# Kernel optimization log

Hardware: AMD Instinct MI355X
Metric: run time of the kernel (lower is better)

The kernel has to match this reference:

```python
import jax, jax.numpy as jnp
import numpy as np

T, B, E = 2048, 2, 256
H = 8
D = E // H


def setup_inputs() -> dict:
    key = jax.random.key(0)
    ks = jax.random.split(key, 10)
    s = 1.0 / np.sqrt(E)
    return {
        "query": jax.random.normal(ks[0], (T, B, E), jnp.float32),
        "attn_bias": jax.random.normal(ks[1], (B, T, T), jnp.float32),
        "Wq": jax.random.normal(ks[2], (E, E), jnp.float32) * s,
        "bq": jax.random.normal(ks[3], (E,), jnp.float32) * 0.02,
        "Wk": jax.random.normal(ks[4], (E, E), jnp.float32) * s,
        "bk": jax.random.normal(ks[5], (E,), jnp.float32) * 0.02,
        "Wv": jax.random.normal(ks[6], (E, E), jnp.float32) * s,
        "bv": jax.random.normal(ks[7], (E,), jnp.float32) * 0.02,
        "Wo": jax.random.normal(ks[8], (E, E), jnp.float32) * s,
        "bo": jax.random.normal(ks[9], (E,), jnp.float32) * 0.02,
    }


def reference(query, attn_bias, Wq, bq, Wk, bk, Wv, bv, Wo, bo):
    # query: [T, B, E] (seq-first). Self-attention: k,v also projected from query.
    t, b, e = query.shape
    scaling = 1.0 / np.sqrt(D)
    q = (query @ Wq.T + bq) * scaling          # [T,B,E]
    k = query @ Wk.T + bk                      # [T,B,E]
    v = query @ Wv.T + bv                      # [T,B,E]
    q = q.reshape(t, b, H, D)
    k = k.reshape(t, b, H, D)
    v = v.reshape(t, b, H, D)
    # raw scores + per-batch additive bias broadcast across heads
    scores = jnp.einsum("tbhd,sbhd->bhts", q, k) + attn_bias[:, None, :, :]
    attn_weights = jax.nn.softmax(scores, axis=-1)  # [B,H,T,S]
    attn = jnp.einsum("bhts,sbhd->tbhd", attn_weights, v).reshape(t, b, e)
    return attn @ Wo.T + bo  # [T,B,E]
```

## Files before the change

kernel.cpp:

```cpp
#include <hip/hip_runtime.h>
#include <hip/hip_bf16.h>

#define T_DIM 2048
#define B_DIM 2
#define E_DIM 256
#define H_DIM 8
#define D_DIM 32
#define M_DIM (T_DIM*B_DIM)
#define SPLIT 4
#define S_CHUNK (T_DIM/SPLIT)

typedef __bf16 bf16x8 __attribute__((ext_vector_type(8)));
typedef __bf16 bf16x4 __attribute__((ext_vector_type(4)));
typedef __bf16 bf16x2 __attribute__((ext_vector_type(2)));
typedef float  f32x4  __attribute__((ext_vector_type(4)));

static __device__ __forceinline__ float fexp2(float x) {
#if __has_builtin(__builtin_amdgcn_exp2f)
    return __builtin_amdgcn_exp2f(x);
#else
    return exp2f(x);
#endif
}

__global__ __launch_bounds__(256)
void qkv_kernel(const float* __restrict__ X,
                const float* __restrict__ Wq, const float* __restrict__ Wk, const float* __restrict__ Wv,
                const float* __restrict__ bq, const float* __restrict__ bk, const float* __restrict__ bv,
                __bf16* __restrict__ qh, __bf16* __restrict__ kperm, __bf16* __restrict__ vperm) {
    __shared__ __align__(16) __bf16 Xs[64][136];
    __shared__ __align__(16) __bf16 Ws[64][136];
    const int m0 = blockIdx.x * 64;
    const int which = blockIdx.y >> 2;
    const int n0 = (blockIdx.y & 3) * 64;
    const float* W = (which == 0) ? Wq : (which == 1) ? Wk : Wv;
    const float* bias = (which == 0) ? bq : (which == 1) ? bk : bv;
    const int tid = threadIdx.x;
    const int wid = tid >> 6, lane = tid & 63;
    const int wm = (wid & 1) * 32, wn = (wid >> 1) * 32;
    const int lr = lane & 15, lg = lane >> 4;

    f32x4 acc[2][2] = {};
    for (int kc = 0; kc < 2; ++kc) {
        for (int c = tid; c < 2048; c += 256) {
            int row = c >> 5, col = (c & 31) * 4;
            float4 xv = *(const float4*)&X[(size_t)(m0 + row) * E_DIM + kc * 128 + col];
            float4 wv = *(const float4*)&W[(size_t)(n0 + row) * E_DIM + kc * 128 + col];
            bf16x4 xb, wb;
            xb[0] = (__bf16)xv.x; xb[1] = (__bf16)xv.y; xb[2] = (__bf16)xv.z; xb[3] = (__bf16)xv.w;
            wb[0] = (__bf16)wv.x; wb[1] = (__bf16)wv.y; wb[2] = (__bf16)wv.z; wb[3] = (__bf16)wv.w;
            *(bf16x4*)&Xs[row][col] = xb;
            *(bf16x4*)&Ws[row][col] = wb;
        }
        __syncthreads();
#pragma unroll
        for (int ks = 0; ks < 4; ++ks) {
            bf16x8 a0 = *(const bf16x8*)&Xs[wm + lr][ks * 32 + lg * 8];
            bf16x8 a1 = *(const bf16x8*)&Xs[wm + 16 + lr][ks * 32 + lg * 8];
            bf16x8 b0 = *(const bf16x8*)&Ws[wn + lr][ks * 32 + lg * 8];
            bf16x8 b1 = *(const bf16x8*)&Ws[wn + 16 + lr][ks * 32 + lg * 8];
            acc[0][0] = __builtin_amdgcn_mfma_f32_16x16x32_bf16(a0, b0, acc[0][0], 0, 0, 0);
            acc[0][1] = __builtin_amdgcn_mfma_f32_16x16x32_bf16(a0, b1, acc[0][1], 0, 0, 0);
            acc[1][0] = __builtin_amdgcn_mfma_f32_16x16x32_bf16(a1, b0, acc[1][0], 0, 0, 0);
            acc[1][1] = __builtin_amdgcn_mfma_f32_16x16x32_bf16(a1, b1, acc[1][1], 0, 0, 0);
        }
        __syncthreads();
    }
    const float scale = 0.17677669529663687f * 1.4426950408889634f;
#pragma unroll
    for (int mt = 0; mt < 2; ++mt) {
#pragma unroll
        for (int nt = 0; nt < 2; ++nt) {
            int n = n0 + wn + nt * 16 + lr;
            float bb = bias[n];
            int h = n >> 5, d = n & 31;
#pragma unroll
            for (int r = 0; r < 4; ++r) {
                int m = m0 + wm + mt * 16 + lg * 4 + r;
                int t = m >> 1, b = m & 1;
                float v = acc[mt][nt][r] + bb;
                if (which == 0) {
                    v *= scale;
                    qh[((size_t)(b * H_DIM + h) * T_DIM + t) * D_DIM + d] = (__bf16)v;
                } else if (which == 1) {
                    int til = t >> 6, s6 = t & 63;
                    int ntk = ((s6 >> 5) << 1) | ((s6 >> 2) & 1);
                    int lrk = (((s6 >> 3) & 3) << 2) | (s6 & 3);
                    int lanek = ((d >> 3) << 4) | lrk;
                    kperm[((((size_t)(b * H_DIM + h) * 32 + til) * 4 + ntk) * 64 + lanek) * 8 + (d & 7)] = (__bf16)v;
                } else {
                    int til = t >> 6;
                    int ktv = (t >> 5) & 1, lgv = (t >> 3) & 3, elv = t & 7;
                    int jv = ktv * 2 + (d >> 4);
                    int lanev = (lgv << 4) | (d & 15);
                    vperm[((((size_t)(b * H_DIM + h) * 32 + til) * 4 + jv) * 64 + lanev) * 8 + elv] = (__bf16)v;
                }
            }
        }
    }
}

__global__ __launch_bounds__(512, 4)
void attn_kernel(const __bf16* __restrict__ qh, const __bf16* __restrict__ kperm,
                 const __bf16* __restrict__ vperm, const float* __restrict__ attn_bias,
                 __bf16* __restrict__ po, float* __restrict__ pl) {
    __shared__ __align__(16) float Bs[16][516];
    const int lin = blockIdx.x + (T_DIM / 16) * (blockIdx.y + B_DIM * blockIdx.z);
    const int combo = lin & 7;
    const int b  = combo & 1;
    const int sp = combo >> 1;
    const int t0 = (lin >> 3) * 16;
    const int tid = threadIdx.x, wid = tid >> 6, lane = tid & 63;
    const int lr = lane & 15, lg = lane >> 4;
    const int bh = b * H_DIM + wid;
    const int sbase = sp * S_CHUNK;
    const int tb0 = sp * 8;
    const float LOG2E = 1.4426950408889634f;

    {
        const float* bsrc = attn_bias + ((size_t)b * T_DIM + t0) * T_DIM + sbase;
        int r = tid >> 5, c0 = (tid & 31) * 4;
#pragma unroll
        for (int rep = 0; rep < 4; ++rep) {
            float4 v = *(const float4*)&bsrc[(size_t)r * T_DIM + rep * 128 + c0];
            float4 w;
            w.x = (v.x - 12.0f) * LOG2E;
            w.y = (v.y - 12.0f) * LOG2E;
            w.z = (v.z - 12.0f) * LOG2E;
            w.w = (v.w - 12.0f) * LOG2E;
            *(float4*)&Bs[r][rep * 128 + c0] = w;
        }
    }
    __syncthreads();

    bf16x8 qf = *(const bf16x8*)&qh[((size_t)bh * T_DIM + t0 + lr) * D_DIM + lg * 8];
    const __bf16* kpb = kperm + (size_t)bh * T_DIM * D_DIM + (size_t)lane * 8;
    const __bf16* vpb = vperm + (size_t)bh * T_DIM * D_DIM + (size_t)lane * 8;

    bf16x8 ones;
#pragma unroll
    for (int i = 0; i < 8; ++i) ones[i] = (__bf16)1.0f;

    f32x4 o0 = {}, o1 = {};
    f32x4 ol = {};

#pragma unroll
    for (int st = 0; st < 8; ++st) {
        const int til = tb0 + st;

        bf16x8 kf0 = *(const bf16x8*)&kpb[(size_t)(til * 4 + 0) * 512];
        bf16x8 kf1 = *(const bf16x8*)&kpb[(size_t)(til * 4 + 1) * 512];
        bf16x8 kf2 = *(const bf16x8*)&kpb[(size_t)(til * 4 + 2) * 512];
        bf16x8 kf3 = *(const bf16x8*)&kpb[(size_t)(til * 4 + 3) * 512];
        bf16x8 vf0 = *(const bf16x8*)&vpb[(size_t)(til * 4 + 0) * 512];
        bf16x8 vf1 = *(const bf16x8*)&vpb[(size_t)(til * 4 + 1) * 512];
        bf16x8 vf2 = *(const bf16x8*)&vpb[(size_t)(til * 4 + 2) * 512];
        bf16x8 vf3 = *(const bf16x8*)&vpb[(size_t)(til * 4 + 3) * 512];

        f32x4 cb0 = *(const f32x4*)&Bs[lr][st * 64 +  0 + lg * 8 + 0];
        f32x4 cb1 = *(const f32x4*)&Bs[lr][st * 64 +  0 + lg * 8 + 4];
        f32x4 cb2 = *(const f32x4*)&Bs[lr][st * 64 + 32 + lg * 8 + 0];
        f32x4 cb3 = *(const f32x4*)&Bs[lr][st * 64 + 32 + lg * 8 + 4];

        f32x4 sv0 = __builtin_amdgcn_mfma_f32_16x16x32_bf16(kf0, qf, cb0, 0, 0, 0);
        f32x4 sv1 = __builtin_amdgcn_mfma_f32_16x16x32_bf16(kf1, qf, cb1, 0, 0, 0);
        f32x4 sv2 = __builtin_amdgcn_mfma_f32_16x16x32_bf16(kf2, qf, cb2, 0, 0, 0);
        f32x4 sv3 = __builtin_amdgcn_mfma_f32_16x16x32_bf16(kf3, qf, cb3, 0, 0, 0);

        f32x4 e0, e1, e2, e3;
#pragma unroll
        for (int r = 0; r < 4; ++r) {
            e0[r] = fexp2(sv0[r]);
            e1[r] = fexp2(sv1[r]);
            e2[r] = fexp2(sv2[r]);
            e3[r] = fexp2(sv3[r]);
        }

        bf16x8 pf0, pf1;
#pragma unroll
        for (int r = 0; r < 4; ++r) {
            pf0[r] = (__bf16)e0[r]; pf0[4 + r] = (__bf16)e1[r];
            pf1[r] = (__bf16)e2[r]; pf1[4 + r] = (__bf16)e3[r];
        }

        o0 = __builtin_amdgcn_mfma_f32_16x16x32_bf16(pf0, vf0, o0, 0, 0, 0);
        o1 = __builtin_amdgcn_mfma_f32_16x16x32_bf16(pf0, vf1, o1, 0, 0, 0);
        ol = __builtin_amdgcn_mfma_f32_16x16x32_bf16(pf0, ones, ol, 0, 0, 0);
        o0 = __builtin_amdgcn_mfma_f32_16x16x32_bf16(pf1, vf2, o0, 0, 0, 0);
        o1 = __builtin_amdgcn_mfma_f32_16x16x32_bf16(pf1, vf3, o1, 0, 0, 0);
        ol = __builtin_amdgcn_mfma_f32_16x16x32_bf16(pf1, ones, ol, 0, 0, 0);
    }

#pragma unroll
    for (int r = 0; r < 4; ++r) {
        int t = t0 + lg * 4 + r;
        size_t rw = ((size_t)bh * T_DIM + t) * SPLIT + sp;
        bf16x2 w;
        w[0] = (__bf16)o0[r];
        w[1] = (__bf16)o1[r];
        *(bf16x2*)&po[rw * D_DIM + lr * 2] = w;
    }
    if (lr == 0)
        *(f32x4*)&pl[(size_t)sp * (B_DIM * H_DIM * T_DIM) + (size_t)bh * T_DIM + t0 + lg * 4] = ol;
}

__global__ __launch_bounds__(256)
void combine_kernel(const __bf16* __restrict__ po, const float* __restrict__ pl,
                    __bf16* __restrict__ attn) {
    int idx = blockIdx.x * 256 + threadIdx.x;
    int row = idx >> 3, dg = idx & 7;
    int bh = row >> 11, t = row & 2047;
    int b = bh >> 3, h = bh & 7;

    float L = 0.f;
    float a0 = 0.f, a1 = 0.f, b0 = 0.f, b1 = 0.f;
#pragma unroll
    for (int s2 = 0; s2 < SPLIT; ++s2) {
        L += pl[(size_t)s2 * (B_DIM * H_DIM * T_DIM) + row];
        bf16x4 v = *(const bf16x4*)&po[((size_t)row * SPLIT + s2) * D_DIM + dg * 4];
        a0 += (float)v[0];
        b0 += (float)v[1];
        a1 += (float)v[2];
        b1 += (float)v[3];
    }
    float inv = 1.0f / L;
    bf16x2 lo, hi;
    lo[0] = (__bf16)(a0 * inv); lo[1] = (__bf16)(a1 * inv);
    hi[0] = (__bf16)(b0 * inv); hi[1] = (__bf16)(b1 * inv);
    size_t base = ((size_t)(t * B_DIM + b)) * E_DIM + h * D_DIM;
    *(bf16x2*)&attn[base + 2 * dg] = lo;
    *(bf16x2*)&attn[base + 16 + 2 * dg] = hi;
}

__global__ __launch_bounds__(256)
void oproj_kernel(const __bf16* __restrict__ X, const float* __restrict__ Wo,
                  const float* __restrict__ bo, float* __restrict__ out) {
    __shared__ __align__(16) __bf16 Xs[64][136];
    __shared__ __align__(16) __bf16 Ws[64][136];
    const int m0 = blockIdx.x * 64;
    const int n0 = blockIdx.y * 64;
    const int tid = threadIdx.x;
    const int wid = tid >> 6, lane = tid & 63;
    const int wm = (wid & 1) * 32, wn = (wid >> 1) * 32;
    const int lr = lane & 15, lg = lane >> 4;

    f32x4 acc[2][2] = {};
    for (int kc = 0; kc < 2; ++kc) {
        for (int c = tid; c < 1024; c += 256) {
            int row = c >> 4, col = (c & 15) * 8;
            *(bf16x8*)&Xs[row][col] = *(const bf16x8*)&X[(size_t)(m0 + row) * E_DIM + kc * 128 + col];
        }
        for (int c = tid; c < 2048; c += 256) {
            int row = c >> 5, col = (c & 31) * 4;
            float4 wv = *(const float4*)&Wo[(size_t)(n0 + row) * E_DIM + kc * 128 + col];
            bf16x4 wb;
            wb[0] = (__bf16)wv.x; wb[1] = (__bf16)wv.y; wb[2] = (__bf16)wv.z; wb[3] = (__bf16)wv.w;
            *(bf16x4*)&Ws[row][col] = wb;
        }
        __syncthreads();
#pragma unroll
        for (int ks = 0; ks < 4; ++ks) {
            bf16x8 a0 = *(const bf16x8*)&Xs[wm + lr][ks * 32 + lg * 8];
            bf16x8 a1 = *(const bf16x8*)&Xs[wm + 16 + lr][ks * 32 + lg * 8];
            bf16x8 b0 = *(const bf16x8*)&Ws[wn + lr][ks * 32 + lg * 8];
            bf16x8 b1 = *(const bf16x8*)&Ws[wn + 16 + lr][ks * 32 + lg * 8];
            acc[0][0] = __builtin_amdgcn_mfma_f32_16x16x32_bf16(a0, b0, acc[0][0], 0, 0, 0);
            acc[0][1] = __builtin_amdgcn_mfma_f32_16x16x32_bf16(a0, b1, acc[0][1], 0, 0, 0);
            acc[1][0] = __builtin_amdgcn_mfma_f32_16x16x32_bf16(a1, b0, acc[1][0], 0, 0, 0);
            acc[1][1] = __builtin_amdgcn_mfma_f32_16x16x32_bf16(a1, b1, acc[1][1], 0, 0, 0);
        }
        __syncthreads();
    }
#pragma unroll
    for (int mt = 0; mt < 2; ++mt) {
#pragma unroll
        for (int nt = 0; nt < 2; ++nt) {
            int n = n0 + wn + nt * 16 + lr;
            float bb = bo[n];
#pragma unroll
            for (int r = 0; r < 4; ++r) {
                int m = m0 + wm + mt * 16 + lg * 4 + r;
                out[(size_t)m * E_DIM + n] = acc[mt][nt][r] + bb;
            }
        }
    }
}

extern "C" void kernel_launch(void* const* d_in, const int* in_sizes, int n_in,
                              void* d_out, int out_size, void* d_ws, size_t ws_size,
                              hipStream_t stream) {
    const float* query     = (const float*)d_in[0];
    const float* attn_bias = (const float*)d_in[1];
    const float* Wq = (const float*)d_in[2];
    const float* bq = (const float*)d_in[3];
    const float* Wk = (const float*)d_in[4];
    const float* bk = (const float*)d_in[5];
    const float* Wv = (const float*)d_in[6];
    const float* bv = (const float*)d_in[7];
    const float* Wo = (const float*)d_in[8];
    const float* bo = (const float*)d_in[9];
    float* out = (float*)d_out;

    char* ws = (char*)d_ws;
    __bf16* qhp  = (__bf16*)(ws);
    __bf16* kpp  = (__bf16*)(ws + 2097152);
    __bf16* vpp  = (__bf16*)(ws + 4194304);
    __bf16* attn = (__bf16*)(ws + 6291456);
    __bf16* po   = (__bf16*)(ws + 8388608);
    float*  pl   = (float*)(ws + 16777216);

    qkv_kernel<<<dim3(M_DIM / 64, 12), 256, 0, stream>>>(
        query, Wq, Wk, Wv, bq, bk, bv, qhp, kpp, vpp);

    attn_kernel<<<dim3(T_DIM / 16, B_DIM, SPLIT), 512, 0, stream>>>(
        qhp, kpp, vpp, attn_bias, po, pl);
    combine_kernel<<<dim3(B_DIM * H_DIM * T_DIM * 8 / 256), 256, 0, stream>>>(po, pl, attn);

    oproj_kernel<<<dim3(M_DIM / 64, E_DIM / 64), 256, 0, stream>>>(attn, Wo, bo, out);
}
```

Measured before the change: 52.64 us.

## Fuse split-softmax combine into output projection and raise MFMA wave priority

Removes the separate combine kernel. The output-projection kernel now reads the per-split partial outputs and row sums directly, normalises them, and writes the result into its shared-memory X tile. This drops one launch and the round trip of the intermediate attn buffer through global memory. In exchange, the combine work is repeated across the four N-blocks of oproj, so partials are re-read four times. It also wraps the MFMA groups in the attention kernel with s_setprio to favour matrix issue over other waves.

```diff
diff --git a/kernel.cpp b/kernel.cpp
--- a/kernel.cpp
+++ b/kernel.cpp
@@ -9,6 +9,7 @@
 #define M_DIM (T_DIM*B_DIM)
 #define SPLIT 4
 #define S_CHUNK (T_DIM/SPLIT)
+#define BHT (B_DIM*H_DIM*T_DIM)
 
 typedef __bf16 bf16x8 __attribute__((ext_vector_type(8)));
 typedef __bf16 bf16x4 __attribute__((ext_vector_type(4)));
@@ -162,10 +163,12 @@
         f32x4 cb2 = *(const f32x4*)&Bs[lr][st * 64 + 32 + lg * 8 + 0];
         f32x4 cb3 = *(const f32x4*)&Bs[lr][st * 64 + 32 + lg * 8 + 4];
 
+        __builtin_amdgcn_s_setprio(1);
         f32x4 sv0 = __builtin_amdgcn_mfma_f32_16x16x32_bf16(kf0, qf, cb0, 0, 0, 0);
         f32x4 sv1 = __builtin_amdgcn_mfma_f32_16x16x32_bf16(kf1, qf, cb1, 0, 0, 0);
         f32x4 sv2 = __builtin_amdgcn_mfma_f32_16x16x32_bf16(kf2, qf, cb2, 0, 0, 0);
         f32x4 sv3 = __builtin_amdgcn_mfma_f32_16x16x32_bf16(kf3, qf, cb3, 0, 0, 0);
+        __builtin_amdgcn_s_setprio(0);
 
         f32x4 e0, e1, e2, e3;
 #pragma unroll
@@ -183,12 +186,14 @@
             pf1[r] = (__bf16)e2[r]; pf1[4 + r] = (__bf16)e3[r];
         }
 
+        __builtin_amdgcn_s_setprio(1);
         o0 = __builtin_amdgcn_mfma_f32_16x16x32_bf16(pf0, vf0, o0, 0, 0, 0);
         o1 = __builtin_amdgcn_mfma_f32_16x16x32_bf16(pf0, vf1, o1, 0, 0, 0);
         ol = __builtin_amdgcn_mfma_f32_16x16x32_bf16(pf0, ones, ol, 0, 0, 0);
         o0 = __builtin_amdgcn_mfma_f32_16x16x32_bf16(pf1, vf2, o0, 0, 0, 0);
         o1 = __builtin_amdgcn_mfma_f32_16x16x32_bf16(pf1, vf3, o1, 0, 0, 0);
         ol = __builtin_amdgcn_mfma_f32_16x16x32_bf16(pf1, ones, ol, 0, 0, 0);
+        __builtin_amdgcn_s_setprio(0);
     }
 
 #pragma unroll
@@ -201,54 +206,59 @@
         *(bf16x2*)&po[rw * D_DIM + lr * 2] = w;
     }
     if (lr == 0)
-        *(f32x4*)&pl[(size_t)sp * (B_DIM * H_DIM * T_DIM) + (size_t)bh * T_DIM + t0 + lg * 4] = ol;
+        *(f32x4*)&pl[(size_t)sp * BHT + (size_t)bh * T_DIM + t0 + lg * 4] = ol;
 }
 
 __global__ __launch_bounds__(256)
-void combine_kernel(const __bf16* __restrict__ po, const float* __restrict__ pl,
-                    __bf16* __restrict__ attn) {
-    int idx = blockIdx.x * 256 + threadIdx.x;
-    int row = idx >> 3, dg = idx & 7;
-    int bh = row >> 11, t = row & 2047;
-    int b = bh >> 3, h = bh & 7;
-
-    float L = 0.f;
-    float a0 = 0.f, a1 = 0.f, b0 = 0.f, b1 = 0.f;
-#pragma unroll
-    for (int s2 = 0; s2 < SPLIT; ++s2) {
-        L += pl[(size_t)s2 * (B_DIM * H_DIM * T_DIM) + row];
-        bf16x4 v = *(const bf16x4*)&po[((size_t)row * SPLIT + s2) * D_DIM + dg * 4];
-        a0 += (float)v[0];
-        b0 += (float)v[1];
-        a1 += (float)v[2];
-        b1 += (float)v[3];
-    }
-    float inv = 1.0f / L;
-    bf16x2 lo, hi;
-    lo[0] = (__bf16)(a0 * inv); lo[1] = (__bf16)(a1 * inv);
-    hi[0] = (__bf16)(b0 * inv); hi[1] = (__bf16)(b1 * inv);
-    size_t base = ((size_t)(t * B_DIM + b)) * E_DIM + h * D_DIM;
-    *(bf16x2*)&attn[base + 2 * dg] = lo;
-    *(bf16x2*)&attn[base + 16 + 2 * dg] = hi;
-}
-
-__global__ __launch_bounds__(256)
-void oproj_kernel(const __bf16* __restrict__ X, const float* __restrict__ Wo,
-                  const float* __restrict__ bo, float* __restrict__ out) {
+void oproj_kernel(const __bf16* __restrict__ po, const float* __restrict__ pl,
+                  const float* __restrict__ Wo, const float* __restrict__ bo,
+                  float* __restrict__ out) {
     __shared__ __align__(16) __bf16 Xs[64][136];
     __shared__ __align__(16) __bf16 Ws[64][136];
+    __shared__ float invLs[16][32];
     const int m0 = blockIdx.x * 64;
     const int n0 = blockIdx.y * 64;
     const int tid = threadIdx.x;
     const int wid = tid >> 6, lane = tid & 63;
     const int wm = (wid & 1) * 32, wn = (wid >> 1) * 32;
     const int lr = lane & 15, lg = lane >> 4;
+    const int tb = m0 >> 1;
+
+#pragma unroll
+    for (int i = 0; i < 2; ++i) {
+        int idx = tid + i * 256;
+        int bhl = idx >> 5, toff = idx & 31;
+        int row = bhl * T_DIM + tb + toff;
+        float L = pl[row] + pl[BHT + row] + pl[2 * BHT + row] + pl[3 * BHT + row];
+        invLs[bhl][toff] = 1.0f / L;
+    }
+    __syncthreads();
 
     f32x4 acc[2][2] = {};
     for (int kc = 0; kc < 2; ++kc) {
-        for (int c = tid; c < 1024; c += 256) {
-            int row = c >> 4, col = (c & 15) * 8;
-            *(bf16x8*)&Xs[row][col] = *(const bf16x8*)&X[(size_t)(m0 + row) * E_DIM + kc * 128 + col];
+#pragma unroll
+        for (int rep = 0; rep < 4; ++rep) {
+            int c = tid + rep * 256;
+            int m_loc = c >> 4;
+            int rem = c & 15;
+            int h_loc = rem >> 2, eb = rem & 3;
+            int b = m_loc & 1;
+            int h = kc * 4 + h_loc;
+            int bh = b * H_DIM + h;
+            int tl = m_loc >> 1;
+            size_t row = (size_t)bh * T_DIM + tb + tl;
+            const __bf16* src = po + row * (SPLIT * D_DIM) + eb * 8;
+            bf16x8 v0 = *(const bf16x8*)(src);
+            bf16x8 v1 = *(const bf16x8*)(src + D_DIM);
+            bf16x8 v2 = *(const bf16x8*)(src + 2 * D_DIM);
+            bf16x8 v3 = *(const bf16x8*)(src + 3 * D_DIM);
+            float invL = invLs[bh & 15][tl];
+#pragma unroll
+            for (int j = 0; j < 8; ++j) {
+                float s = ((float)v0[j] + (float)v1[j]) + ((float)v2[j] + (float)v3[j]);
+                int d = (j & 1) * 16 + eb * 4 + (j >> 1);
+                Xs[m_loc][h_loc * 32 + d] = (__bf16)(s * invL);
+            }
         }
         for (int c = tid; c < 2048; c += 256) {
             int row = c >> 5, col = (c & 31) * 4;
@@ -305,16 +315,14 @@
     __bf16* qhp  = (__bf16*)(ws);
     __bf16* kpp  = (__bf16*)(ws + 2097152);
     __bf16* vpp  = (__bf16*)(ws + 4194304);
-    __bf16* attn = (__bf16*)(ws + 6291456);
-    __bf16* po   = (__bf16*)(ws + 8388608);
-    float*  pl   = (float*)(ws + 16777216);
+    __bf16* po   = (__bf16*)(ws + 6291456);
+    float*  pl   = (float*)(ws + 14680064);
 
     qkv_kernel<<<dim3(M_DIM / 64, 12), 256, 0, stream>>>(
         query, Wq, Wk, Wv, bq, bk, bv, qhp, kpp, vpp);
 
     attn_kernel<<<dim3(T_DIM / 16, B_DIM, SPLIT), 512, 0, stream>>>(
         qhp, kpp, vpp, attn_bias, po, pl);
-    combine_kernel<<<dim3(B_DIM * H_DIM * T_DIM * 8 / 256), 256, 0, stream>>>(po, pl, attn);
-
-    oproj_kernel<<<dim3(M_DIM / 64, E_DIM / 64), 256, 0, stream>>>(attn, Wo, bo, out);
-}
+
+    oproj_kernel<<<dim3(M_DIM / 64, E_DIM / 64), 256, 0, stream>>>(po, pl, Wo, bo, out);
+}
```

Result: no change. 53.50 us (+1.6%).
